# Kernel tuning notes

Hardware: AMD Instinct MI355X
Metric: run time of the kernel (lower is better)

Reference implementation:

```python
import math
import jax, jax.numpy as jnp
import numpy as np

C = 1024  # n_embd
B, T = 4, 2048
H = 4 * C  # mlp hidden
EPS = 1e-5


def setup_inputs() -> dict:
    key = jax.random.key(0)
    ks = jax.random.split(key, 8)
    s = 0.02
    return {
        "x": jax.random.normal(ks[0], (B, T, C), jnp.float32),
        "ln1_g": jnp.ones((C,), jnp.float32),
        "ln1_b": jnp.zeros((C,), jnp.float32),
        "w_attn": jax.random.normal(ks[1], (C, 3 * C), jnp.float32) * s,
        "b_attn": jnp.zeros((3 * C,), jnp.float32),
        "w_proj": jax.random.normal(ks[2], (C, C), jnp.float32) * s,
        "b_proj": jnp.zeros((C,), jnp.float32),
        "ln2_g": jnp.ones((C,), jnp.float32),
        "ln2_b": jnp.zeros((C,), jnp.float32),
        "w_fc": jax.random.normal(ks[3], (C, H), jnp.float32) * s,
        "b_fc": jnp.zeros((H,), jnp.float32),
        "w_mlp_proj": jax.random.normal(ks[4], (H, C), jnp.float32) * s,
        "b_mlp_proj": jnp.zeros((C,), jnp.float32),
    }


def _layernorm(x, g, b):
    mu = jnp.mean(x, axis=-1, keepdims=True)
    var = jnp.mean(jnp.square(x - mu), axis=-1, keepdims=True)
    return (x - mu) * jax.lax.rsqrt(var + EPS) * g + b


def _new_gelu(x):
    c = math.sqrt(2.0 / math.pi)
    return 0.5 * x * (1.0 + jnp.tanh(c * (x + 0.044715 * x * x * x)))


def reference(x, ln1_g, ln1_b, w_attn, b_attn, w_proj, b_proj,
              ln2_g, ln2_b, w_fc, b_fc, w_mlp_proj, b_mlp_proj):
    # --- attention sublayer (single-head, full-dim, no causal mask) ---
    h = _layernorm(x, ln1_g, ln1_b)
    qkv = h @ w_attn + b_attn              # [B,T,3C]
    q, k, v = jnp.split(qkv, 3, axis=-1)   # each [B,T,C]
    scale = 1.0 / math.sqrt(C)
    att = jnp.einsum("btc,bsc->bts", q, k) * scale  # [B,T,T]
    att = jax.nn.softmax(att, axis=-1)
    y = jnp.einsum("bts,bsc->btc", att, v)
    y = y @ w_proj + b_proj
    x = x + y
    # --- MLP sublayer ---
    h2 = _layernorm(x, ln2_g, ln2_b)
    m = _new_gelu(h2 @ w_fc + b_fc) @ w_mlp_proj + b_mlp_proj
    return x + m
```

## Files before the change

### kernel.cpp

```cpp
#include <hip/hip_runtime.h>

typedef __bf16 bf16;
typedef bf16 bf16x8 __attribute__((ext_vector_type(8)));
typedef bf16 bf16x4 __attribute__((ext_vector_type(4)));
typedef float f32x16 __attribute__((ext_vector_type(16)));

#define C_DIM 1024
#define T_DIM 2048
#define B_DIM 4
#define H_DIM 4096

__device__ inline void gld_lds16(const bf16* g, bf16* l) {
    __builtin_amdgcn_global_load_lds(
        (const __attribute__((address_space(1))) unsigned int*)g,
        (__attribute__((address_space(3))) unsigned int*)l,
        16, 0, 0);
}

__device__ inline float fast_gelu(float u) {
    float k2 = 1.5957691216057308f * u + 0.07135480895843475f * u * u * u;
    float t = __expf(-k2);
    return u * __builtin_amdgcn_rcpf(1.0f + t);
}

template <int EPI, typename OutT>
__launch_bounds__(256, 3)
__global__ void gemm_bt(const bf16* __restrict__ A, int lda, long long sA,
                        const bf16* __restrict__ Bt, int ldb, long long sB,
                        OutT* __restrict__ Cout, int ldc, long long sC,
                        const float* __restrict__ bias,
                        const float* __restrict__ resid, long long sR,
                        float alpha, int K) {
    const int z = blockIdx.z;
    A += (long long)z * sA;
    Bt += (long long)z * sB;
    Cout += (long long)z * sC;
    if (resid) resid += (long long)z * sR;

    const int rowBase = blockIdx.x * 128;
    const int colBase = blockIdx.y * 128;

    __shared__ __align__(16) bf16 As[128 * 64];
    __shared__ __align__(16) bf16 Bs[128 * 64];

    const int tid = threadIdx.x;
    const int w = tid >> 6, lane = tid & 63;
    const int wm = w & 1, wn = w >> 1;
    const int ln31 = lane & 31, lh = lane >> 5;

    const int srow = tid >> 3;
    const int scol = ((tid & 7) ^ (srow & 7)) << 3;
    const bf16* Abase = A + (size_t)(rowBase + srow) * lda + scol;
    const bf16* Bbase = Bt + (size_t)(colBase + srow) * ldb + scol;
    bf16* ldsA = As + (size_t)(w * 64) * 8;
    bf16* ldsB = Bs + (size_t)(w * 64) * 8;

    const int rA = wm * 64 + ln31;
    const int rB = wn * 64 + ln31;
    const int swA = rA & 7, swB = rB & 7;

    f32x16 acc[2][2] = {};

    for (int k0 = 0; k0 < K; k0 += 64) {
        __syncthreads();
#pragma unroll
        for (int t = 0; t < 4; t++) {
            gld_lds16(Abase + (size_t)(t * 32) * lda + k0, ldsA + t * 2048);
            gld_lds16(Bbase + (size_t)(t * 32) * ldb + k0, ldsB + t * 2048);
        }
        __syncthreads();
#pragma unroll
        for (int ks = 0; ks < 4; ks++) {
            bf16x8 af[2], bfv[2];
            const int cc = (ks << 1) | lh;
#pragma unroll
            for (int i = 0; i < 2; i++)
                af[i] = *(const bf16x8*)(As + (rA + i * 32) * 64 + ((cc ^ swA) << 3));
#pragma unroll
            for (int j = 0; j < 2; j++)
                bfv[j] = *(const bf16x8*)(Bs + (rB + j * 32) * 64 + ((cc ^ swB) << 3));
#pragma unroll
            for (int i = 0; i < 2; i++)
#pragma unroll
                for (int j = 0; j < 2; j++)
                    acc[i][j] = __builtin_amdgcn_mfma_f32_32x32x16_bf16(af[i], bfv[j], acc[i][j], 0, 0, 0);
        }
    }

    float bval[2];
#pragma unroll
    for (int j = 0; j < 2; j++)
        bval[j] = bias ? bias[colBase + wn * 64 + j * 32 + ln31] : 0.0f;
#pragma unroll
    for (int i = 0; i < 2; i++) {
        const int rtile = rowBase + wm * 64 + i * 32 + 4 * lh;
#pragma unroll
        for (int j = 0; j < 2; j++) {
            const int col = colBase + wn * 64 + j * 32 + ln31;
#pragma unroll
            for (int reg = 0; reg < 16; reg++) {
                const int row = rtile + (reg & 3) + 8 * (reg >> 2);
                float v = acc[i][j][reg] * alpha + bval[j];
                if constexpr (EPI == 1) {
                    v = fast_gelu(v);
                }
                if constexpr (EPI == 2) {
                    v += resid[(size_t)row * ldc + col];
                }
                Cout[(size_t)row * ldc + col] = (OutT)v;
            }
        }
    }
}

__launch_bounds__(256)
__global__ void ln_kernel(const float* __restrict__ x, const float* __restrict__ g,
                          const float* __restrict__ b, bf16* __restrict__ out) {
    __shared__ float red[4];
    const int row = blockIdx.x;
    const int tid = threadIdx.x;
    const float4* xr = (const float4*)(x + (size_t)row * C_DIM);
    float4 v = xr[tid];
    float s = v.x + v.y + v.z + v.w;
#pragma unroll
    for (int m = 32; m; m >>= 1) s += __shfl_xor(s, m, 64);
    if ((tid & 63) == 0) red[tid >> 6] = s;
    __syncthreads();
    const float mu = (red[0] + red[1] + red[2] + red[3]) * (1.0f / C_DIM);
    const float dx = v.x - mu, dy = v.y - mu, dz = v.z - mu, dw = v.w - mu;
    float q = dx * dx + dy * dy + dz * dz + dw * dw;
#pragma unroll
    for (int m = 32; m; m >>= 1) q += __shfl_xor(q, m, 64);
    __syncthreads();
    if ((tid & 63) == 0) red[tid >> 6] = q;
    __syncthreads();
    const float var = (red[0] + red[1] + red[2] + red[3]) * (1.0f / C_DIM);
    const float rs = rsqrtf(var + 1e-5f);
    const float4 gg = ((const float4*)g)[tid];
    const float4 bb = ((const float4*)b)[tid];
    bf16x4 o;
    o[0] = (bf16)(dx * rs * gg.x + bb.x);
    o[1] = (bf16)(dy * rs * gg.y + bb.y);
    o[2] = (bf16)(dz * rs * gg.z + bb.z);
    o[3] = (bf16)(dw * rs * gg.w + bb.w);
    ((bf16x4*)(out + (size_t)row * C_DIM))[tid] = o;
}

__launch_bounds__(256)
__global__ void softmax_kernel(const bf16* __restrict__ S, bf16* __restrict__ P) {
    __shared__ float red[4];
    const size_t base = (size_t)blockIdx.x * T_DIM;
    const int tid = threadIdx.x;
    bf16x8 sv = ((const bf16x8*)(S + base))[tid];
    float e[8];
#pragma unroll
    for (int i = 0; i < 8; i++) e[i] = (float)sv[i];
    float mx = e[0];
#pragma unroll
    for (int i = 1; i < 8; i++) mx = fmaxf(mx, e[i]);
#pragma unroll
    for (int m = 32; m; m >>= 1) mx = fmaxf(mx, __shfl_xor(mx, m, 64));
    if ((tid & 63) == 0) red[tid >> 6] = mx;
    __syncthreads();
    mx = fmaxf(fmaxf(red[0], red[1]), fmaxf(red[2], red[3]));
    float s = 0.0f;
#pragma unroll
    for (int i = 0; i < 8; i++) {
        e[i] = __expf(e[i] - mx);
        s += e[i];
    }
#pragma unroll
    for (int m = 32; m; m >>= 1) s += __shfl_xor(s, m, 64);
    __syncthreads();
    if ((tid & 63) == 0) red[tid >> 6] = s;
    __syncthreads();
    const float inv = 1.0f / (red[0] + red[1] + red[2] + red[3]);
    bf16x8 p;
#pragma unroll
    for (int i = 0; i < 8; i++) p[i] = (bf16)(e[i] * inv);
    ((bf16x8*)(P + base))[tid] = p;
}

__global__ void transpose_f2b_all(const float* __restrict__ s0, bf16* __restrict__ d0,
                                  const float* __restrict__ s1, bf16* __restrict__ d1,
                                  const float* __restrict__ s2, bf16* __restrict__ d2,
                                  const float* __restrict__ s3, bf16* __restrict__ d3) {
    __shared__ float tile[32][33];
    int id = blockIdx.x;
    const float* src;
    bf16* dst;
    int R, Cc, local;
    if (id < 3072)       { src = s0; dst = d0; R = 1024; Cc = 3072; local = id; }
    else if (id < 4096)  { src = s1; dst = d1; R = 1024; Cc = 1024; local = id - 3072; }
    else if (id < 8192)  { src = s2; dst = d2; R = 1024; Cc = 4096; local = id - 4096; }
    else                 { src = s3; dst = d3; R = 4096; Cc = 1024; local = id - 8192; }
    const int tilesX = Cc >> 5;
    const int bx = (local % tilesX) * 32;
    const int by = (local / tilesX) * 32;
    const int tx = threadIdx.x, ty = threadIdx.y;
    for (int i = ty; i < 32; i += 8)
        tile[i][tx] = src[(size_t)(by + i) * Cc + bx + tx];
    __syncthreads();
    for (int i = ty; i < 32; i += 8)
        dst[(size_t)(bx + i) * R + by + tx] = (bf16)tile[tx][i];
}

__global__ void transpose_b2b(const bf16* __restrict__ src, int ldsrc, long long sstride,
                              bf16* __restrict__ dst, long long dstride, int R) {
    __shared__ bf16 tile[32][33];
    src += (long long)blockIdx.z * sstride;
    dst += (long long)blockIdx.z * dstride;
    const int bx = blockIdx.x * 32;
    const int by = blockIdx.y * 32;
    const int tx = threadIdx.x, ty = threadIdx.y;
    for (int i = ty; i < 32; i += 8)
        tile[i][tx] = src[(size_t)(by + i) * ldsrc + bx + tx];
    __syncthreads();
    for (int i = ty; i < 32; i += 8)
        dst[(size_t)(bx + i) * R + by + tx] = tile[tx][i];
}

extern "C" void kernel_launch(void* const* d_in, const int* in_sizes, int n_in,
                              void* d_out, int out_size, void* d_ws, size_t ws_size,
                              hipStream_t stream) {
    const float* x      = (const float*)d_in[0];
    const float* ln1_g  = (const float*)d_in[1];
    const float* ln1_b  = (const float*)d_in[2];
    const float* w_attn = (const float*)d_in[3];
    const float* b_attn = (const float*)d_in[4];
    const float* w_proj = (const float*)d_in[5];
    const float* b_proj = (const float*)d_in[6];
    const float* ln2_g  = (const float*)d_in[7];
    const float* ln2_b  = (const float*)d_in[8];
    const float* w_fc   = (const float*)d_in[9];
    const float* b_fc   = (const float*)d_in[10];
    const float* w_mlp  = (const float*)d_in[11];
    const float* b_mlp  = (const float*)d_in[12];
    float* out = (float*)d_out;

    const int M = B_DIM * T_DIM;

    char* base = (char*)d_ws;
    size_t off = 0;
    auto alloc = [&](size_t bytes) -> char* {
        char* p = base + off;
        off += (bytes + 255) & ~(size_t)255;
        return p;
    };
    bf16* wT_attn = (bf16*)alloc((size_t)3072 * 1024 * 2);
    bf16* wT_proj = (bf16*)alloc((size_t)1024 * 1024 * 2);
    bf16* wT_fc   = (bf16*)alloc((size_t)4096 * 1024 * 2);
    bf16* wT_mlp  = (bf16*)alloc((size_t)1024 * 4096 * 2);
    bf16* h       = (bf16*)alloc((size_t)M * 1024 * 2);
    bf16* qkv     = (bf16*)alloc((size_t)M * 3072 * 2);
    bf16* vT      = (bf16*)alloc((size_t)B_DIM * 1024 * 2048 * 2);
    bf16* S       = (bf16*)alloc((size_t)B_DIM * 2048 * 2048 * 2);
    bf16* P       = (bf16*)alloc((size_t)B_DIM * 2048 * 2048 * 2);
    bf16* y       = (bf16*)alloc((size_t)M * 1024 * 2);
    float* x2     = (float*)alloc((size_t)M * 1024 * 4);
    bf16* act     = (bf16*)S;

    const dim3 tb(32, 8);

    transpose_f2b_all<<<12288, tb, 0, stream>>>(w_attn, wT_attn, w_proj, wT_proj,
                                                w_fc, wT_fc, w_mlp, wT_mlp);

    ln_kernel<<<M, 256, 0, stream>>>(x, ln1_g, ln1_b, h);

    gemm_bt<0, bf16><<<dim3(64, 24, 1), 256, 0, stream>>>(
        h, 1024, 0, wT_attn, 1024, 0, qkv, 3072, 0, b_attn, nullptr, 0, 1.0f, 1024);

    transpose_b2b<<<dim3(1024 / 32, 2048 / 32, B_DIM), tb, 0, stream>>>(
        qkv + 2 * C_DIM, 3072, (long long)T_DIM * 3072, vT, (long long)C_DIM * T_DIM, T_DIM);

    gemm_bt<0, bf16><<<dim3(16, 16, B_DIM), 256, 0, stream>>>(
        qkv, 3072, (long long)T_DIM * 3072,
        qkv + C_DIM, 3072, (long long)T_DIM * 3072,
        S, 2048, (long long)T_DIM * T_DIM, nullptr, nullptr, 0, 0.03125f, 1024);

    softmax_kernel<<<B_DIM * T_DIM, 256, 0, stream>>>(S, P);

    gemm_bt<0, bf16><<<dim3(16, 8, B_DIM), 256, 0, stream>>>(
        P, 2048, (long long)T_DIM * T_DIM,
        vT, 2048, (long long)C_DIM * T_DIM,
        y, 1024, (long long)T_DIM * C_DIM, nullptr, nullptr, 0, 1.0f, 2048);

    gemm_bt<2, float><<<dim3(64, 8, 1), 256, 0, stream>>>(
        y, 1024, 0, wT_proj, 1024, 0, x2, 1024, 0, b_proj, x, 0, 1.0f, 1024);

    ln_kernel<<<M, 256, 0, stream>>>(x2, ln2_g, ln2_b, h);

    gemm_bt<1, bf16><<<dim3(64, 32, 1), 256, 0, stream>>>(
        h, 1024, 0, wT_fc, 1024, 0, act, 4096, 0, b_fc, nullptr, 0, 1.0f, 1024);

    gemm_bt<2, float><<<dim3(64, 8, 1), 256, 0, stream>>>(
        act, 4096, 0, wT_mlp, 4096, 0, out, 1024, 0, b_mlp, x2, 0, 1.0f, 4096);
}
```

Baseline: 515.7 us.

## Fold softmax exp into QK GEMM epilogue and defer normalization to PV GEMM

The QK^T GEMM epilogue now writes exp(scaled score) directly, without subtracting the row max. A light rowsum kernel replaces the full softmax pass. The PV GEMM epilogue then divides each output row by its row sum. This drops the write of a separate probability matrix and the max reduction, but exp can overflow if scores ever exceed the fp32/bf16 range.

```diff
diff --git a/kernel.cpp b/kernel.cpp
--- a/kernel.cpp
+++ b/kernel.cpp
@@ -107,6 +107,12 @@
                 if constexpr (EPI == 2) {
                     v += resid[(size_t)row * ldc + col];
                 }
+                if constexpr (EPI == 3) {
+                    v = __expf(v);
+                }
+                if constexpr (EPI == 4) {
+                    v *= __builtin_amdgcn_rcpf(resid[row]);
+                }
                 Cout[(size_t)row * ldc + col] = (OutT)v;
             }
         }
@@ -147,38 +153,19 @@
 }
 
 __launch_bounds__(256)
-__global__ void softmax_kernel(const bf16* __restrict__ S, bf16* __restrict__ P) {
+__global__ void rowsum_kernel(const bf16* __restrict__ E, float* __restrict__ rowsum) {
     __shared__ float red[4];
     const size_t base = (size_t)blockIdx.x * T_DIM;
     const int tid = threadIdx.x;
-    bf16x8 sv = ((const bf16x8*)(S + base))[tid];
-    float e[8];
-#pragma unroll
-    for (int i = 0; i < 8; i++) e[i] = (float)sv[i];
-    float mx = e[0];
-#pragma unroll
-    for (int i = 1; i < 8; i++) mx = fmaxf(mx, e[i]);
-#pragma unroll
-    for (int m = 32; m; m >>= 1) mx = fmaxf(mx, __shfl_xor(mx, m, 64));
-    if ((tid & 63) == 0) red[tid >> 6] = mx;
-    __syncthreads();
-    mx = fmaxf(fmaxf(red[0], red[1]), fmaxf(red[2], red[3]));
+    bf16x8 sv = ((const bf16x8*)(E + base))[tid];
     float s = 0.0f;
 #pragma unroll
-    for (int i = 0; i < 8; i++) {
-        e[i] = __expf(e[i] - mx);
-        s += e[i];
-    }
+    for (int i = 0; i < 8; i++) s += (float)sv[i];
 #pragma unroll
     for (int m = 32; m; m >>= 1) s += __shfl_xor(s, m, 64);
-    __syncthreads();
     if ((tid & 63) == 0) red[tid >> 6] = s;
     __syncthreads();
-    const float inv = 1.0f / (red[0] + red[1] + red[2] + red[3]);
-    bf16x8 p;
-#pragma unroll
-    for (int i = 0; i < 8; i++) p[i] = (bf16)(e[i] * inv);
-    ((bf16x8*)(P + base))[tid] = p;
+    if (tid == 0) rowsum[blockIdx.x] = red[0] + red[1] + red[2] + red[3];
 }
 
 __global__ void transpose_f2b_all(const float* __restrict__ s0, bf16* __restrict__ d0,
@@ -254,11 +241,13 @@
     bf16* h       = (bf16*)alloc((size_t)M * 1024 * 2);
     bf16* qkv     = (bf16*)alloc((size_t)M * 3072 * 2);
     bf16* vT      = (bf16*)alloc((size_t)B_DIM * 1024 * 2048 * 2);
-    bf16* S       = (bf16*)alloc((size_t)B_DIM * 2048 * 2048 * 2);
-    bf16* P       = (bf16*)alloc((size_t)B_DIM * 2048 * 2048 * 2);
+    bf16* E       = (bf16*)alloc((size_t)B_DIM * 2048 * 2048 * 2);
+    bf16* spare   = (bf16*)alloc((size_t)B_DIM * 2048 * 2048 * 2);
     bf16* y       = (bf16*)alloc((size_t)M * 1024 * 2);
     float* x2     = (float*)alloc((size_t)M * 1024 * 4);
-    bf16* act     = (bf16*)S;
+    float* rowsum = (float*)alloc((size_t)M * 4);
+    bf16* act     = (bf16*)E;
+    (void)spare;
 
     const dim3 tb(32, 8);
 
@@ -273,17 +262,17 @@
     transpose_b2b<<<dim3(1024 / 32, 2048 / 32, B_DIM), tb, 0, stream>>>(
         qkv + 2 * C_DIM, 3072, (long long)T_DIM * 3072, vT, (long long)C_DIM * T_DIM, T_DIM);
 
-    gemm_bt<0, bf16><<<dim3(16, 16, B_DIM), 256, 0, stream>>>(
+    gemm_bt<3, bf16><<<dim3(16, 16, B_DIM), 256, 0, stream>>>(
         qkv, 3072, (long long)T_DIM * 3072,
         qkv + C_DIM, 3072, (long long)T_DIM * 3072,
-        S, 2048, (long long)T_DIM * T_DIM, nullptr, nullptr, 0, 0.03125f, 1024);
-
-    softmax_kernel<<<B_DIM * T_DIM, 256, 0, stream>>>(S, P);
-
-    gemm_bt<0, bf16><<<dim3(16, 8, B_DIM), 256, 0, stream>>>(
-        P, 2048, (long long)T_DIM * T_DIM,
+        E, 2048, (long long)T_DIM * T_DIM, nullptr, nullptr, 0, 0.03125f, 1024);
+
+    rowsum_kernel<<<M, 256, 0, stream>>>(E, rowsum);
+
+    gemm_bt<4, bf16><<<dim3(16, 8, B_DIM), 256, 0, stream>>>(
+        E, 2048, (long long)T_DIM * T_DIM,
         vT, 2048, (long long)C_DIM * T_DIM,
-        y, 1024, (long long)T_DIM * C_DIM, nullptr, nullptr, 0, 1.0f, 2048);
+        y, 1024, (long long)T_DIM * C_DIM, nullptr, rowsum, T_DIM, 1.0f, 2048);
 
     gemm_bt<2, float><<<dim3(64, 8, 1), 256, 0, stream>>>(
         y, 1024, 0, wT_proj, 1024, 0, x2, 1024, 0, b_proj, x, 0, 1.0f, 1024);
```

After: 525.5 us. Within noise of the previous version (+1.9%).
